# Performance work log

Hardware: AMD Instinct MI355X
Metric: run time of the kernel (lower is better)

The kernel has to match this reference:

```python
import jax, jax.numpy as jnp
import numpy as np

N_NODES = 50000
N_EDGES = 600000
N_PAIRS = 200000
F_ATOM = 64
F_PAIR = 32
HID = 128
N_LAYERS = 3
EPS = 1e-5


def setup_inputs() -> dict:
    key = jax.random.key(0)
    ks = jax.random.split(key, 24)
    d = {}
    d["atom_features"] = jax.random.normal(ks[0], (N_NODES, F_ATOM), jnp.float32)
    d["edge_index"] = jax.random.randint(ks[1], (2, N_EDGES), 0, N_NODES)
    d["pair_indices"] = jax.random.randint(ks[2], (N_PAIRS, 2), 0, N_NODES)
    d["pair_features"] = jax.random.normal(ks[3], (N_PAIRS, F_PAIR), jnp.float32)
    # atom embedding linear
    d["embed_W"] = jax.random.normal(ks[4], (F_ATOM, HID), jnp.float32) / np.sqrt(F_ATOM)
    d["embed_b"] = jnp.zeros((HID,), jnp.float32)
    # stacked GCNConv weights [L, HID, HID]
    d["conv_W"] = jax.random.normal(ks[5], (N_LAYERS, HID, HID), jnp.float32) / np.sqrt(HID)
    d["conv_b"] = jnp.zeros((N_LAYERS, HID), jnp.float32)
    # BatchNorm (eval mode: running stats)
    d["bn_gamma"] = jnp.ones((N_LAYERS, HID), jnp.float32)
    d["bn_beta"] = jnp.zeros((N_LAYERS, HID), jnp.float32)
    d["bn_mean"] = jax.random.normal(ks[6], (N_LAYERS, HID), jnp.float32) * 0.1
    d["bn_var"] = jax.random.uniform(ks[7], (N_LAYERS, HID), jnp.float32, 0.5, 1.5)
    # pair MLP: Linear(2H+Fp -> H), Linear(H -> H//2), Linear(H//2 -> 1)
    din1 = 2 * HID + F_PAIR
    d["mlp_W1"] = jax.random.normal(ks[8], (din1, HID), jnp.float32) / np.sqrt(din1)
    d["mlp_b1"] = jnp.zeros((HID,), jnp.float32)
    d["mlp_W2"] = jax.random.normal(ks[9], (HID, HID // 2), jnp.float32) / np.sqrt(HID)
    d["mlp_b2"] = jnp.zeros((HID // 2,), jnp.float32)
    d["mlp_W3"] = jax.random.normal(ks[10], (HID // 2, 1), jnp.float32) / np.sqrt(HID // 2)
    d["mlp_b3"] = jnp.zeros((1,), jnp.float32)
    return d


def _gcn_conv(x, W, b, row, col, deg_inv_sqrt):
    # PyG GCNConv: x' = W x, then symmetric-normalized sum aggregation (self-loops
    # already folded into row/col/deg_inv_sqrt).
    h = x @ W  # [N, H]
    norm = deg_inv_sqrt[row] * deg_inv_sqrt[col]  # [E']
    msg = h[col] * norm[:, None]  # [E', H] gather
    out = jax.ops.segment_sum(msg, row, num_segments=x.shape[0])  # scatter-add
    return out + b


def reference(atom_features, edge_index, pair_indices, pair_features,
              embed_W, embed_b, conv_W, conv_b,
              bn_gamma, bn_beta, bn_mean, bn_var,
              mlp_W1, mlp_b1, mlp_W2, mlp_b2, mlp_W3, mlp_b3):
    n = atom_features.shape[0]
    # add self loops once (same for every layer)
    loop = jnp.arange(n, dtype=edge_index.dtype)
    row = jnp.concatenate([edge_index[0], loop])
    col = jnp.concatenate([edge_index[1], loop])
    deg = jax.ops.segment_sum(jnp.ones_like(row, dtype=jnp.float32), row, num_segments=n)
    deg_inv_sqrt = jnp.where(deg > 0, jax.lax.rsqrt(deg), 0.0)

    x = atom_features @ embed_W + embed_b  # [N, H]
    for i in range(N_LAYERS):
        x = _gcn_conv(x, conv_W[i], conv_b[i], row, col, deg_inv_sqrt)
        # BatchNorm1d, eval mode (running stats)
        x = (x - bn_mean[i]) * jax.lax.rsqrt(bn_var[i] + EPS) * bn_gamma[i] + bn_beta[i]
        x = jax.nn.relu(x)
        # dropout: identity in eval mode

    p0 = x[pair_indices[:, 0]]  # [P, H]
    p1 = x[pair_indices[:, 1]]  # [P, H]
    z = jnp.concatenate([p0, p1, pair_features], axis=1)  # [P, 2H+Fp]
    z = jax.nn.relu(z @ mlp_W1 + mlp_b1)
    z = jax.nn.relu(z @ mlp_W2 + mlp_b2)
    return z @ mlp_W3 + mlp_b3  # [P, 1]
```

## Files before the change

kernel.cpp:

```cpp
#include <hip/hip_runtime.h>
#include <hip/hip_bf16.h>
#include <stdint.h>

#define NN 50000
#define NE 600000
#define NP 200000
#define SCAN_CHUNK 1024
#define NB_SCAN ((NN + SCAN_CHUNK - 1) / SCAN_CHUNK)

typedef __attribute__((ext_vector_type(8))) short short8;
typedef __attribute__((ext_vector_type(4))) float f32x4;

static __device__ __forceinline__ unsigned short f2bf(float f) {
  union { float f; unsigned u; } a; a.f = f;
  unsigned r = a.u + 0x7fff + ((a.u >> 16) & 1);
  return (unsigned short)(r >> 16);
}
static __device__ __forceinline__ float bf2f(unsigned short h) {
  union { unsigned u; float f; } a; a.u = ((unsigned)h) << 16;
  return a.f;
}
static __device__ __forceinline__ float lo16f(unsigned w) {
  union { unsigned u; float f; } a; a.u = w << 16; return a.f;
}
static __device__ __forceinline__ float hi16f(unsigned w) {
  union { unsigned u; float f; } a; a.u = w & 0xffff0000u; return a.f;
}


__global__ void count_kernel(const int* __restrict__ rows, int* __restrict__ counts) {
  int e = blockIdx.x * 256 + threadIdx.x;
  if (e < NE) atomicAdd(&counts[rows[e]], 1);
}

__global__ void dis_kernel(const int* __restrict__ counts, float* __restrict__ dis) {
  int i = blockIdx.x * 256 + threadIdx.x;
  if (i < NN) dis[i] = rsqrtf((float)counts[i] + 1.0f);
}

__global__ __launch_bounds__(256) void scan_partial(const int* __restrict__ counts,
                                                    int* __restrict__ bsum) {
  const int b = blockIdx.x, t = threadIdx.x;
  const int base = b * SCAN_CHUNK;
  int s = 0;
  for (int j = t; j < SCAN_CHUNK; j += 256) {
    int i = base + j;
    if (i < NN) s += counts[i];
  }
  __shared__ int red[4];
#pragma unroll
  for (int off = 32; off; off >>= 1) s += __shfl_down(s, off);
  if ((t & 63) == 0) red[t >> 6] = s;
  __syncthreads();
  if (t == 0) bsum[b] = red[0] + red[1] + red[2] + red[3];
}

__global__ void scan_mid(const int* __restrict__ bsum, int* __restrict__ bbase) {
  int t = threadIdx.x;
  int v = (t < NB_SCAN) ? bsum[t] : 0;
  int orig = v;
#pragma unroll
  for (int off = 1; off < 64; off <<= 1) {
    int u = __shfl_up(v, off);
    if (t >= off) v += u;
  }
  if (t < NB_SCAN) bbase[t] = v - orig;
}

__global__ __launch_bounds__(256) void scan_final(const int* __restrict__ counts,
                                                  const int* __restrict__ bbase,
                                                  int* __restrict__ row_ptr,
                                                  int* __restrict__ cursor) {
  const int b = blockIdx.x, t = threadIdx.x;
  const int i0 = b * SCAN_CHUNK + t * 4;
  int c[4]; int s = 0;
#pragma unroll
  for (int r = 0; r < 4; ++r) { int i = i0 + r; c[r] = (i < NN) ? counts[i] : 0; s += c[r]; }
  __shared__ int sc[256];
  sc[t] = s;
  __syncthreads();
  for (int off = 1; off < 256; off <<= 1) {
    int add = (t >= off) ? sc[t - off] : 0;
    __syncthreads();
    sc[t] += add;
    __syncthreads();
  }
  int run = bbase[b] + sc[t] - s;
#pragma unroll
  for (int r = 0; r < 4; ++r) {
    int i = i0 + r;
    if (i < NN) { row_ptr[i] = run; cursor[i] = run; run += c[r]; }
  }
  if (b == 0 && t == 0) row_ptr[NN] = NE;
}

__global__ void fill_kernel(const int* __restrict__ rows, const int* __restrict__ cols,
                            int* __restrict__ cursor, int* __restrict__ csr_col) {
  int e = blockIdx.x * 256 + threadIdx.x;
  if (e < NE) {
    int r = rows[e];
    int pos = atomicAdd(&cursor[r], 1);
    csr_col[pos] = cols[e];
  }
}


__global__ void prep_w(const float* __restrict__ embW, const float* __restrict__ convW,
                       const float* __restrict__ W1, const float* __restrict__ W2,
                       unsigned short* __restrict__ embT_hi, unsigned short* __restrict__ embT_lo,
                       unsigned short* __restrict__ convT_hi, unsigned short* __restrict__ convT_lo,
                       unsigned short* __restrict__ W1T, unsigned short* __restrict__ W2T) {
  int idx = blockIdx.x * 256 + threadIdx.x;
  if (idx < 8192) {
    int n = idx >> 6, k = idx & 63;
    float v = embW[(size_t)k * 128 + n];
    unsigned short h = f2bf(v);
    embT_hi[idx] = h;
    embT_lo[idx] = f2bf(v - bf2f(h));
  } else if (idx < 8192 + 49152) {
    int i2 = idx - 8192;
    int l = i2 >> 14, n = (i2 >> 7) & 127, k = i2 & 127;
    float v = convW[(size_t)l * 16384 + (size_t)k * 128 + n];
    unsigned short h = f2bf(v);
    convT_hi[i2] = h;
    convT_lo[i2] = f2bf(v - bf2f(h));
  } else if (idx < 8192 + 49152 + 36864) {
    int i3 = idx - 57344;
    int n = i3 / 288, k = i3 % 288;
    W1T[i3] = f2bf(W1[(size_t)k * 128 + n]);
  } else if (idx < 8192 + 49152 + 36864 + 8192) {
    int i4 = idx - 94208;
    int n = i4 >> 7, k = i4 & 127;
    W2T[i4] = f2bf(W2[(size_t)k * 64 + n]);
  }
}


__global__ __launch_bounds__(256) void agg3_kernel(const unsigned short* __restrict__ xsb,
    const int* __restrict__ row_ptr, const int* __restrict__ csr_col,
    const float* __restrict__ dis, unsigned short* __restrict__ y_bf) {
  const int t = threadIdx.x;
  const int n = blockIdx.x * 4 + (t >> 6);
  if (n >= NN) return;
  const int c = t & 63;
  const unsigned* xsw = (const unsigned*)xsb;

  unsigned wself = xsw[(size_t)n * 64 + c];
  float a0 = lo16f(wself), a1 = hi16f(wself);

  const int s = row_ptr[n], e = row_ptr[n + 1];
  int j = s;
  for (; j + 8 <= e; j += 8) {
    int cc[8]; unsigned ww[8];
#pragma unroll
    for (int q = 0; q < 8; ++q) cc[q] = csr_col[j + q];
#pragma unroll
    for (int q = 0; q < 8; ++q) ww[q] = xsw[(size_t)cc[q] * 64 + c];
#pragma unroll
    for (int q = 0; q < 8; ++q) { a0 += lo16f(ww[q]); a1 += hi16f(ww[q]); }
  }
  if (j + 4 <= e) {
    int cc[4]; unsigned ww[4];
#pragma unroll
    for (int q = 0; q < 4; ++q) cc[q] = csr_col[j + q];
#pragma unroll
    for (int q = 0; q < 4; ++q) ww[q] = xsw[(size_t)cc[q] * 64 + c];
#pragma unroll
    for (int q = 0; q < 4; ++q) { a0 += lo16f(ww[q]); a1 += hi16f(ww[q]); }
    j += 4;
  }
  for (; j < e; ++j) {
    unsigned w0 = xsw[(size_t)csr_col[j] * 64 + c];
    a0 += lo16f(w0);
    a1 += hi16f(w0);
  }
  float dv = dis[n];
  unsigned short h0 = f2bf(dv * a0), h1 = f2bf(dv * a1);
  ((unsigned*)y_bf)[(size_t)n * 64 + c] = (unsigned)h0 | ((unsigned)h1 << 16);
}


template<int K, int MODE, bool AF32>
__global__ __launch_bounds__(256) void mfma_gemm(
    const float* __restrict__ Af,
    const unsigned short* __restrict__ Ab,
    const unsigned short* __restrict__ BThi, const unsigned short* __restrict__ BTlo,
    const float* __restrict__ bias, const float* __restrict__ dis,
    const float* __restrict__ g, const float* __restrict__ be,
    const float* __restrict__ mn, const float* __restrict__ vr,
    unsigned short* __restrict__ outb, int M) {
  const int tid  = threadIdx.x;
  const int lane = tid & 63;
  const int w    = tid >> 6;
  const int l15  = lane & 15;
  const int khi  = (lane >> 4) * 8;
  const int rowb = blockIdx.x * 128 + w * 32;

  int ar[2];
#pragma unroll
  for (int rt = 0; rt < 2; ++rt) {
    int r = rowb + rt * 16 + l15;
    ar[rt] = (r < M) ? r : M - 1;
  }

  f32x4 acc[2][8];
#pragma unroll
  for (int rt = 0; rt < 2; ++rt)
#pragma unroll
    for (int ct = 0; ct < 8; ++ct) acc[rt][ct] = (f32x4){0.f, 0.f, 0.f, 0.f};

#pragma unroll
  for (int kb = 0; kb < K; kb += 32) {
    short8 ahi[2], alo[2];
#pragma unroll
    for (int rt = 0; rt < 2; ++rt) {
      if constexpr (AF32) {
        const float* asrc = Af + (size_t)ar[rt] * K + kb + khi;
        float4 va0 = *(const float4*)(asrc);
        float4 va1 = *(const float4*)(asrc + 4);
        float av[8] = {va0.x, va0.y, va0.z, va0.w, va1.x, va1.y, va1.z, va1.w};
#pragma unroll
        for (int j = 0; j < 8; ++j) {
          unsigned short h = f2bf(av[j]);
          ahi[rt][j] = (short)h;
          alo[rt][j] = (short)f2bf(av[j] - bf2f(h));
        }
      } else {
        ahi[rt] = *(const short8*)(Ab + (size_t)ar[rt] * K + kb + khi);
      }
    }
#pragma unroll
    for (int ct = 0; ct < 8; ++ct) {
      size_t woff = (size_t)(ct * 16 + l15) * K + kb + khi;
      short8 bhi = *(const short8*)(BThi + woff);
      short8 blo = *(const short8*)(BTlo + woff);
#pragma unroll
      for (int rt = 0; rt < 2; ++rt) {
        acc[rt][ct] = __builtin_amdgcn_mfma_f32_16x16x32_bf16(ahi[rt], bhi, acc[rt][ct], 0, 0, 0);
        if constexpr (AF32)
          acc[rt][ct] = __builtin_amdgcn_mfma_f32_16x16x32_bf16(alo[rt], bhi, acc[rt][ct], 0, 0, 0);
        acc[rt][ct] = __builtin_amdgcn_mfma_f32_16x16x32_bf16(ahi[rt], blo, acc[rt][ct], 0, 0, 0);
      }
    }
  }

#pragma unroll
  for (int rt = 0; rt < 2; ++rt) {
    const int orow0 = rowb + rt * 16 + (lane >> 4) * 4;
    float dv[4];
    if constexpr (MODE != 2) {
#pragma unroll
      for (int r = 0; r < 4; ++r) dv[r] = (orow0 + r < M) ? dis[orow0 + r] : 0.f;
    }
#pragma unroll
    for (int ct = 0; ct < 8; ++ct) {
      int col = ct * 16 + l15;
      float bb = bias[col];
      float scale = 1.f, shift = 0.f;
      if constexpr (MODE >= 1) {
        float inv = rsqrtf(vr[col] + 1e-5f);
        scale = g[col] * inv;
        shift = be[col] - mn[col] * scale;
      }
#pragma unroll
      for (int r = 0; r < 4; ++r) {
        int orow = orow0 + r;
        if (orow < M) {
          float v = acc[rt][ct][r] + bb;
          if constexpr (MODE >= 1) v = fmaxf(v * scale + shift, 0.f);
          if constexpr (MODE != 2) v *= dv[r];
          outb[(size_t)orow * 128 + col] = f2bf(v);
        }
      }
    }
  }
}


__global__ __launch_bounds__(256, 3) void mlp2_kernel(
    const unsigned short* __restrict__ xb, const int* __restrict__ pairs,
    const float* __restrict__ pf,
    const unsigned short* __restrict__ W1T, const float* __restrict__ b1,
    const unsigned short* __restrict__ W2T, const float* __restrict__ b2,
    const float* __restrict__ W3, const float* __restrict__ b3,
    float* __restrict__ out) {
  __shared__ unsigned short H1[128 * 136];

  const int tid  = threadIdx.x;
  const int lane = tid & 63;
  const int w    = tid >> 6;
  const int pb   = blockIdx.x * 128;
  const int rowbase = w * 32;
  const int l15  = lane & 15;
  const int khi  = (lane >> 4) * 8;
  const int rq   = (lane >> 4) * 4;

  int gp0 = pb + rowbase + l15;       if (gp0 >= NP) gp0 = NP - 1;
  int gp1 = pb + rowbase + 16 + l15;  if (gp1 >= NP) gp1 = NP - 1;
  const int2 pr0 = ((const int2*)pairs)[gp0];
  const int2 pr1 = ((const int2*)pairs)[gp1];

  short8 af[18];
#pragma unroll
  for (int kb = 0; kb < 4; ++kb) {
    af[kb]     = *(const short8*)(xb + (size_t)pr0.x * 128 + kb * 32 + khi);
    af[4 + kb] = *(const short8*)(xb + (size_t)pr0.y * 128 + kb * 32 + khi);
    af[9 + kb]     = *(const short8*)(xb + (size_t)pr1.x * 128 + kb * 32 + khi);
    af[9 + 4 + kb] = *(const short8*)(xb + (size_t)pr1.y * 128 + kb * 32 + khi);
  }
  {
    const float* q0 = pf + (size_t)gp0 * 32 + khi;
    const float* q1 = pf + (size_t)gp1 * 32 + khi;
    float4 u0 = *(const float4*)(q0), u1 = *(const float4*)(q0 + 4);
    float4 v0 = *(const float4*)(q1), v1 = *(const float4*)(q1 + 4);
    float fu[8] = {u0.x, u0.y, u0.z, u0.w, u1.x, u1.y, u1.z, u1.w};
    float fv[8] = {v0.x, v0.y, v0.z, v0.w, v1.x, v1.y, v1.z, v1.w};
#pragma unroll
    for (int j = 0; j < 8; ++j) {
      af[8][j]  = (short)f2bf(fu[j]);
      af[17][j] = (short)f2bf(fv[j]);
    }
  }

  f32x4 acc[2][8];
#pragma unroll
  for (int p = 0; p < 2; ++p)
#pragma unroll
    for (int c = 0; c < 8; ++c) acc[p][c] = (f32x4){0.f, 0.f, 0.f, 0.f};

#pragma unroll
  for (int kb = 0; kb < 9; ++kb) {
    const unsigned short* wrow = W1T + (size_t)kb * 32 + khi;
#pragma unroll
    for (int ct = 0; ct < 8; ++ct) {
      short8 bfrag = *(const short8*)(wrow + (size_t)(ct * 16 + l15) * 288);
      acc[0][ct] = __builtin_amdgcn_mfma_f32_16x16x32_bf16(af[kb], bfrag, acc[0][ct], 0, 0, 0);
      acc[1][ct] = __builtin_amdgcn_mfma_f32_16x16x32_bf16(af[9 + kb], bfrag, acc[1][ct], 0, 0, 0);
    }
  }

#pragma unroll
  for (int ct = 0; ct < 8; ++ct) {
    float bv = b1[ct * 16 + l15];
    int col = ct * 16 + l15;
#pragma unroll
    for (int p = 0; p < 2; ++p) {
#pragma unroll
      for (int r = 0; r < 4; ++r) {
        int row = rowbase + p * 16 + rq + r;
        float v = fmaxf(acc[p][ct][r] + bv, 0.f);
        H1[row * 136 + col] = f2bf(v);
      }
    }
  }
  __syncthreads();

  f32x4 acc2[2][4];
#pragma unroll
  for (int p = 0; p < 2; ++p)
#pragma unroll
    for (int c = 0; c < 4; ++c) acc2[p][c] = (f32x4){0.f, 0.f, 0.f, 0.f};

#pragma unroll
  for (int kb = 0; kb < 4; ++kb) {
    int ko = kb * 32 + khi;
    short8 a0 = *(const short8*)&H1[(rowbase + l15) * 136 + ko];
    short8 a1 = *(const short8*)&H1[(rowbase + 16 + l15) * 136 + ko];
    const unsigned short* wrow = W2T + (size_t)ko;
#pragma unroll
    for (int ct = 0; ct < 4; ++ct) {
      short8 bfrag = *(const short8*)(wrow + (size_t)(ct * 16 + l15) * 128);
      acc2[0][ct] = __builtin_amdgcn_mfma_f32_16x16x32_bf16(a0, bfrag, acc2[0][ct], 0, 0, 0);
      acc2[1][ct] = __builtin_amdgcn_mfma_f32_16x16x32_bf16(a1, bfrag, acc2[1][ct], 0, 0, 0);
    }
  }

  float w3v[4], b2v[4];
#pragma unroll
  for (int ct = 0; ct < 4; ++ct) {
    w3v[ct] = W3[ct * 16 + l15];
    b2v[ct] = b2[ct * 16 + l15];
  }
  float b3v = b3[0];
#pragma unroll
  for (int p = 0; p < 2; ++p) {
#pragma unroll
    for (int r = 0; r < 4; ++r) {
      float s = 0.f;
#pragma unroll
      for (int ct = 0; ct < 4; ++ct) {
        float h2 = fmaxf(acc2[p][ct][r] + b2v[ct], 0.f);
        s += h2 * w3v[ct];
      }
      s += __shfl_xor(s, 1);
      s += __shfl_xor(s, 2);
      s += __shfl_xor(s, 4);
      s += __shfl_xor(s, 8);
      int row = pb + rowbase + p * 16 + rq + r;
      if (l15 == 0 && row < NP) out[row] = s + b3v;
    }
  }
}


extern "C" void kernel_launch(void* const* d_in, const int* in_sizes, int n_in,
                              void* d_out, int out_size, void* d_ws, size_t ws_size,
                              hipStream_t stream) {
  (void)in_sizes; (void)n_in; (void)out_size; (void)ws_size;
  const float* atom  = (const float*)d_in[0];
  const int*   eidx  = (const int*)d_in[1];
  const int*   pairs = (const int*)d_in[2];
  const float* pfeat = (const float*)d_in[3];
  const float* embW  = (const float*)d_in[4];
  const float* embB  = (const float*)d_in[5];
  const float* convW = (const float*)d_in[6];
  const float* convB = (const float*)d_in[7];
  const float* bng   = (const float*)d_in[8];
  const float* bnb   = (const float*)d_in[9];
  const float* bnm   = (const float*)d_in[10];
  const float* bnv   = (const float*)d_in[11];
  const float* W1    = (const float*)d_in[12];
  const float* b1    = (const float*)d_in[13];
  const float* W2    = (const float*)d_in[14];
  const float* b2    = (const float*)d_in[15];
  const float* W3    = (const float*)d_in[16];
  const float* b3    = (const float*)d_in[17];
  float* out = (float*)d_out;

  uintptr_t base = (uintptr_t)d_ws;
  auto alloc = [&](size_t bytes) -> uintptr_t {
    uintptr_t p = base;
    base += (bytes + 255) & ~(size_t)255;
    return p;
  };
  int*   counts  = (int*)alloc((size_t)NN * 4);
  int*   row_ptr = (int*)alloc((size_t)(NN + 1) * 4);
  int*   cursor  = (int*)alloc((size_t)NN * 4);
  int*   csr_col = (int*)alloc((size_t)NE * 4);
  float* dis     = (float*)alloc((size_t)NN * 4);
  int*   bsum    = (int*)alloc(64 * 4);
  int*   bbase   = (int*)alloc(64 * 4);
  unsigned short* xs_bf = (unsigned short*)alloc((size_t)NN * 128 * 2);
  unsigned short* y_bf  = (unsigned short*)alloc((size_t)NN * 128 * 2);
  unsigned short* embT_hi  = (unsigned short*)alloc(8192 * 2);
  unsigned short* embT_lo  = (unsigned short*)alloc(8192 * 2);
  unsigned short* convT_hi = (unsigned short*)alloc(49152 * 2);
  unsigned short* convT_lo = (unsigned short*)alloc(49152 * 2);
  unsigned short* W1T      = (unsigned short*)alloc(36864 * 2);
  unsigned short* W2T      = (unsigned short*)alloc(8192 * 2);

  const int* erow = eidx;
  const int* ecol = eidx + NE;

  hipMemsetAsync(counts, 0, (size_t)NN * 4, stream);
  count_kernel<<<(NE + 255) / 256, 256, 0, stream>>>(erow, counts);
  dis_kernel<<<(NN + 255) / 256, 256, 0, stream>>>(counts, dis);
  scan_partial<<<NB_SCAN, 256, 0, stream>>>(counts, bsum);
  scan_mid<<<1, 64, 0, stream>>>(bsum, bbase);
  scan_final<<<NB_SCAN, 256, 0, stream>>>(counts, bbase, row_ptr, cursor);
  fill_kernel<<<(NE + 255) / 256, 256, 0, stream>>>(erow, ecol, cursor, csr_col);
  prep_w<<<(102400 + 255) / 256, 256, 0, stream>>>(embW, convW, W1, W2,
                                                   embT_hi, embT_lo, convT_hi, convT_lo,
                                                   W1T, W2T);

  mfma_gemm<64, 0, true><<<(NN + 127) / 128, 256, 0, stream>>>(
      atom, nullptr, embT_hi, embT_lo, embB, dis,
      nullptr, nullptr, nullptr, nullptr, xs_bf, NN);

  for (int l = 0; l < 3; ++l) {
    agg3_kernel<<<(NN + 3) / 4, 256, 0, stream>>>(xs_bf, row_ptr, csr_col, dis, y_bf);
    if (l < 2) {
      mfma_gemm<128, 1, false><<<(NN + 127) / 128, 256, 0, stream>>>(
          nullptr, y_bf,
          convT_hi + (size_t)l * 16384, convT_lo + (size_t)l * 16384,
          convB + (size_t)l * 128, dis,
          bng + (size_t)l * 128, bnb + (size_t)l * 128,
          bnm + (size_t)l * 128, bnv + (size_t)l * 128, xs_bf, NN);
    } else {
      mfma_gemm<128, 2, false><<<(NN + 127) / 128, 256, 0, stream>>>(
          nullptr, y_bf,
          convT_hi + (size_t)l * 16384, convT_lo + (size_t)l * 16384,
          convB + (size_t)l * 128, nullptr,
          bng + (size_t)l * 128, bnb + (size_t)l * 128,
          bnm + (size_t)l * 128, bnv + (size_t)l * 128, xs_bf, NN);
    }
  }

  mlp2_kernel<<<(NP + 127) / 128, 256, 0, stream>>>(xs_bf, pairs, pfeat,
                                                    W1T, b1, W2T, b2, W3, b3, out);
}
```

Before: 351.8 us.

## Fuse neighbor aggregation with layer GEMM via LDS tile per 64-node block

Merges the per-layer aggregation kernel and the following MFMA GEMM into one kernel. Each 512-thread block aggregates 64 nodes into a swizzled LDS tile, then runs the bf16 hi/lo MFMA GEMM with BatchNorm/ReLU on that tile. This removes the intermediate y buffer round-trip through global memory and three kernel launches. It uses ping-pong buffers between layers, at the cost of lower occupancy and an aggregation phase serialized per block.

```diff
diff --git a/kernel.cpp b/kernel.cpp
--- a/kernel.cpp
+++ b/kernel.cpp
@@ -136,59 +136,12 @@
 }
 
 
-__global__ __launch_bounds__(256) void agg3_kernel(const unsigned short* __restrict__ xsb,
-    const int* __restrict__ row_ptr, const int* __restrict__ csr_col,
-    const float* __restrict__ dis, unsigned short* __restrict__ y_bf) {
-  const int t = threadIdx.x;
-  const int n = blockIdx.x * 4 + (t >> 6);
-  if (n >= NN) return;
-  const int c = t & 63;
-  const unsigned* xsw = (const unsigned*)xsb;
-
-  unsigned wself = xsw[(size_t)n * 64 + c];
-  float a0 = lo16f(wself), a1 = hi16f(wself);
-
-  const int s = row_ptr[n], e = row_ptr[n + 1];
-  int j = s;
-  for (; j + 8 <= e; j += 8) {
-    int cc[8]; unsigned ww[8];
-#pragma unroll
-    for (int q = 0; q < 8; ++q) cc[q] = csr_col[j + q];
-#pragma unroll
-    for (int q = 0; q < 8; ++q) ww[q] = xsw[(size_t)cc[q] * 64 + c];
-#pragma unroll
-    for (int q = 0; q < 8; ++q) { a0 += lo16f(ww[q]); a1 += hi16f(ww[q]); }
-  }
-  if (j + 4 <= e) {
-    int cc[4]; unsigned ww[4];
-#pragma unroll
-    for (int q = 0; q < 4; ++q) cc[q] = csr_col[j + q];
-#pragma unroll
-    for (int q = 0; q < 4; ++q) ww[q] = xsw[(size_t)cc[q] * 64 + c];
-#pragma unroll
-    for (int q = 0; q < 4; ++q) { a0 += lo16f(ww[q]); a1 += hi16f(ww[q]); }
-    j += 4;
-  }
-  for (; j < e; ++j) {
-    unsigned w0 = xsw[(size_t)csr_col[j] * 64 + c];
-    a0 += lo16f(w0);
-    a1 += hi16f(w0);
-  }
-  float dv = dis[n];
-  unsigned short h0 = f2bf(dv * a0), h1 = f2bf(dv * a1);
-  ((unsigned*)y_bf)[(size_t)n * 64 + c] = (unsigned)h0 | ((unsigned)h1 << 16);
-}
-
-
-template<int K, int MODE, bool AF32>
-__global__ __launch_bounds__(256) void mfma_gemm(
+__global__ __launch_bounds__(256) void embed_gemm(
     const float* __restrict__ Af,
-    const unsigned short* __restrict__ Ab,
     const unsigned short* __restrict__ BThi, const unsigned short* __restrict__ BTlo,
     const float* __restrict__ bias, const float* __restrict__ dis,
-    const float* __restrict__ g, const float* __restrict__ be,
-    const float* __restrict__ mn, const float* __restrict__ vr,
     unsigned short* __restrict__ outb, int M) {
+  const int K = 64;
   const int tid  = threadIdx.x;
   const int lane = tid & 63;
   const int w    = tid >> 6;
@@ -214,19 +167,15 @@
     short8 ahi[2], alo[2];
 #pragma unroll
     for (int rt = 0; rt < 2; ++rt) {
-      if constexpr (AF32) {
-        const float* asrc = Af + (size_t)ar[rt] * K + kb + khi;
-        float4 va0 = *(const float4*)(asrc);
-        float4 va1 = *(const float4*)(asrc + 4);
-        float av[8] = {va0.x, va0.y, va0.z, va0.w, va1.x, va1.y, va1.z, va1.w};
-#pragma unroll
-        for (int j = 0; j < 8; ++j) {
-          unsigned short h = f2bf(av[j]);
-          ahi[rt][j] = (short)h;
-          alo[rt][j] = (short)f2bf(av[j] - bf2f(h));
-        }
-      } else {
-        ahi[rt] = *(const short8*)(Ab + (size_t)ar[rt] * K + kb + khi);
+      const float* asrc = Af + (size_t)ar[rt] * K + kb + khi;
+      float4 va0 = *(const float4*)(asrc);
+      float4 va1 = *(const float4*)(asrc + 4);
+      float av[8] = {va0.x, va0.y, va0.z, va0.w, va1.x, va1.y, va1.z, va1.w};
+#pragma unroll
+      for (int j = 0; j < 8; ++j) {
+        unsigned short h = f2bf(av[j]);
+        ahi[rt][j] = (short)h;
+        alo[rt][j] = (short)f2bf(av[j] - bf2f(h));
       }
     }
 #pragma unroll
@@ -237,8 +186,7 @@
 #pragma unroll
       for (int rt = 0; rt < 2; ++rt) {
         acc[rt][ct] = __builtin_amdgcn_mfma_f32_16x16x32_bf16(ahi[rt], bhi, acc[rt][ct], 0, 0, 0);
-        if constexpr (AF32)
-          acc[rt][ct] = __builtin_amdgcn_mfma_f32_16x16x32_bf16(alo[rt], bhi, acc[rt][ct], 0, 0, 0);
+        acc[rt][ct] = __builtin_amdgcn_mfma_f32_16x16x32_bf16(alo[rt], bhi, acc[rt][ct], 0, 0, 0);
         acc[rt][ct] = __builtin_amdgcn_mfma_f32_16x16x32_bf16(ahi[rt], blo, acc[rt][ct], 0, 0, 0);
       }
     }
@@ -248,29 +196,124 @@
   for (int rt = 0; rt < 2; ++rt) {
     const int orow0 = rowb + rt * 16 + (lane >> 4) * 4;
     float dv[4];
-    if constexpr (MODE != 2) {
-#pragma unroll
-      for (int r = 0; r < 4; ++r) dv[r] = (orow0 + r < M) ? dis[orow0 + r] : 0.f;
-    }
+#pragma unroll
+    for (int r = 0; r < 4; ++r) dv[r] = (orow0 + r < M) ? dis[orow0 + r] : 0.f;
 #pragma unroll
     for (int ct = 0; ct < 8; ++ct) {
       int col = ct * 16 + l15;
       float bb = bias[col];
-      float scale = 1.f, shift = 0.f;
-      if constexpr (MODE >= 1) {
-        float inv = rsqrtf(vr[col] + 1e-5f);
-        scale = g[col] * inv;
-        shift = be[col] - mn[col] * scale;
-      }
 #pragma unroll
       for (int r = 0; r < 4; ++r) {
         int orow = orow0 + r;
         if (orow < M) {
-          float v = acc[rt][ct][r] + bb;
-          if constexpr (MODE >= 1) v = fmaxf(v * scale + shift, 0.f);
-          if constexpr (MODE != 2) v *= dv[r];
+          float v = (acc[rt][ct][r] + bb) * dv[r];
           outb[(size_t)orow * 128 + col] = f2bf(v);
         }
+      }
+    }
+  }
+}
+
+
+template<int MODE>
+__global__ __launch_bounds__(512) void fused_layer(
+    const unsigned short* __restrict__ xsb,
+    const int* __restrict__ row_ptr, const int* __restrict__ csr_col,
+    const float* __restrict__ dis,
+    const unsigned short* __restrict__ BThi, const unsigned short* __restrict__ BTlo,
+    const float* __restrict__ bias,
+    const float* __restrict__ g, const float* __restrict__ be,
+    const float* __restrict__ mn, const float* __restrict__ vr,
+    unsigned short* __restrict__ outb) {
+  __shared__ unsigned ytile[64 * 64];
+
+  const int tid  = threadIdx.x;
+  const int w    = tid >> 6;
+  const int lane = tid & 63;
+  const int nb   = blockIdx.x * 64;
+  const unsigned* xsw = (const unsigned*)xsb;
+
+  for (int i = 0; i < 8; ++i) {
+    const int rloc = w * 8 + i;
+    const int n = nb + rloc;
+    float a0 = 0.f, a1 = 0.f;
+    if (n < NN) {
+      unsigned ws = xsw[(size_t)n * 64 + lane];
+      a0 = lo16f(ws); a1 = hi16f(ws);
+      const int s = row_ptr[n], e = row_ptr[n + 1];
+      int j = s;
+      for (; j + 8 <= e; j += 8) {
+        int cc[8]; unsigned ww[8];
+#pragma unroll
+        for (int q = 0; q < 8; ++q) cc[q] = csr_col[j + q];
+#pragma unroll
+        for (int q = 0; q < 8; ++q) ww[q] = xsw[(size_t)cc[q] * 64 + lane];
+#pragma unroll
+        for (int q = 0; q < 8; ++q) { a0 += lo16f(ww[q]); a1 += hi16f(ww[q]); }
+      }
+      if (j + 4 <= e) {
+        int cc[4]; unsigned ww[4];
+#pragma unroll
+        for (int q = 0; q < 4; ++q) cc[q] = csr_col[j + q];
+#pragma unroll
+        for (int q = 0; q < 4; ++q) ww[q] = xsw[(size_t)cc[q] * 64 + lane];
+#pragma unroll
+        for (int q = 0; q < 4; ++q) { a0 += lo16f(ww[q]); a1 += hi16f(ww[q]); }
+        j += 4;
+      }
+      for (; j < e; ++j) {
+        unsigned w0 = xsw[(size_t)csr_col[j] * 64 + lane];
+        a0 += lo16f(w0);
+        a1 += hi16f(w0);
+      }
+      float dv = dis[n];
+      a0 *= dv; a1 *= dv;
+    }
+    unsigned short h0 = f2bf(a0), h1 = f2bf(a1);
+    ytile[rloc * 64 + (lane ^ ((rloc & 15) << 2))] = (unsigned)h0 | ((unsigned)h1 << 16);
+  }
+  __syncthreads();
+
+  const int l15  = lane & 15;
+  const int k4   = lane >> 4;
+  const int r    = (w & 3) * 16 + l15;
+  const int colh = (w >> 2) * 64;
+  const int rsw  = (r & 15) << 2;
+
+  f32x4 acc[4];
+#pragma unroll
+  for (int ct = 0; ct < 4; ++ct) acc[ct] = (f32x4){0.f, 0.f, 0.f, 0.f};
+
+#pragma unroll
+  for (int kb = 0; kb < 4; ++kb) {
+    int q = kb * 4 + k4;
+    int chunk = q ^ (rsw >> 2);
+    short8 afrag = *(const short8*)&ytile[r * 64 + chunk * 4];
+#pragma unroll
+    for (int ct = 0; ct < 4; ++ct) {
+      size_t woff = (size_t)(colh + ct * 16 + l15) * 128 + kb * 32 + k4 * 8;
+      short8 bhi = *(const short8*)(BThi + woff);
+      short8 blo = *(const short8*)(BTlo + woff);
+      acc[ct] = __builtin_amdgcn_mfma_f32_16x16x32_bf16(afrag, bhi, acc[ct], 0, 0, 0);
+      acc[ct] = __builtin_amdgcn_mfma_f32_16x16x32_bf16(afrag, blo, acc[ct], 0, 0, 0);
+    }
+  }
+
+  const int orow0 = nb + (w & 3) * 16 + k4 * 4;
+#pragma unroll
+  for (int ct = 0; ct < 4; ++ct) {
+    int col = colh + ct * 16 + l15;
+    float bb = bias[col];
+    float inv = rsqrtf(vr[col] + 1e-5f);
+    float scale = g[col] * inv;
+    float shift = be[col] - mn[col] * scale;
+#pragma unroll
+    for (int rr = 0; rr < 4; ++rr) {
+      int orow = orow0 + rr;
+      if (orow < NN) {
+        float v = fmaxf((acc[ct][rr] + bb) * scale + shift, 0.f);
+        if constexpr (MODE == 1) v *= dis[orow];
+        outb[(size_t)orow * 128 + col] = f2bf(v);
       }
     }
   }
@@ -440,8 +483,8 @@
   float* dis     = (float*)alloc((size_t)NN * 4);
   int*   bsum    = (int*)alloc(64 * 4);
   int*   bbase   = (int*)alloc(64 * 4);
-  unsigned short* xs_bf = (unsigned short*)alloc((size_t)NN * 128 * 2);
-  unsigned short* y_bf  = (unsigned short*)alloc((size_t)NN * 128 * 2);
+  unsigned short* xsA = (unsigned short*)alloc((size_t)NN * 128 * 2);
+  unsigned short* xsB = (unsigned short*)alloc((size_t)NN * 128 * 2);
   unsigned short* embT_hi  = (unsigned short*)alloc(8192 * 2);
   unsigned short* embT_lo  = (unsigned short*)alloc(8192 * 2);
   unsigned short* convT_hi = (unsigned short*)alloc(49152 * 2);
@@ -463,29 +506,23 @@
                                                    embT_hi, embT_lo, convT_hi, convT_lo,
                                                    W1T, W2T);
 
-  mfma_gemm<64, 0, true><<<(NN + 127) / 128, 256, 0, stream>>>(
-      atom, nullptr, embT_hi, embT_lo, embB, dis,
-      nullptr, nullptr, nullptr, nullptr, xs_bf, NN);
-
-  for (int l = 0; l < 3; ++l) {
-    agg3_kernel<<<(NN + 3) / 4, 256, 0, stream>>>(xs_bf, row_ptr, csr_col, dis, y_bf);
-    if (l < 2) {
-      mfma_gemm<128, 1, false><<<(NN + 127) / 128, 256, 0, stream>>>(
-          nullptr, y_bf,
-          convT_hi + (size_t)l * 16384, convT_lo + (size_t)l * 16384,
-          convB + (size_t)l * 128, dis,
-          bng + (size_t)l * 128, bnb + (size_t)l * 128,
-          bnm + (size_t)l * 128, bnv + (size_t)l * 128, xs_bf, NN);
-    } else {
-      mfma_gemm<128, 2, false><<<(NN + 127) / 128, 256, 0, stream>>>(
-          nullptr, y_bf,
-          convT_hi + (size_t)l * 16384, convT_lo + (size_t)l * 16384,
-          convB + (size_t)l * 128, nullptr,
-          bng + (size_t)l * 128, bnb + (size_t)l * 128,
-          bnm + (size_t)l * 128, bnv + (size_t)l * 128, xs_bf, NN);
-    }
-  }
-
-  mlp2_kernel<<<(NP + 127) / 128, 256, 0, stream>>>(xs_bf, pairs, pfeat,
+  embed_gemm<<<(NN + 127) / 128, 256, 0, stream>>>(
+      atom, embT_hi, embT_lo, embB, dis, xsA, NN);
+
+  const int NBLK = (NN + 63) / 64;
+  fused_layer<1><<<NBLK, 512, 0, stream>>>(
+      xsA, row_ptr, csr_col, dis,
+      convT_hi + 0 * 16384, convT_lo + 0 * 16384, convB + 0 * 128,
+      bng + 0 * 128, bnb + 0 * 128, bnm + 0 * 128, bnv + 0 * 128, xsB);
+  fused_layer<1><<<NBLK, 512, 0, stream>>>(
+      xsB, row_ptr, csr_col, dis,
+      convT_hi + 1 * 16384, convT_lo + 1 * 16384, convB + 1 * 128,
+      bng + 1 * 128, bnb + 1 * 128, bnm + 1 * 128, bnv + 1 * 128, xsA);
+  fused_layer<2><<<NBLK, 512, 0, stream>>>(
+      xsA, row_ptr, csr_col, dis,
+      convT_hi + 2 * 16384, convT_lo + 2 * 16384, convB + 2 * 128,
+      bng + 2 * 128, bnb + 2 * 128, bnm + 2 * 128, bnv + 2 * 128, xsB);
+
+  mlp2_kernel<<<(NP + 127) / 128, 256, 0, stream>>>(xsB, pairs, pfeat,
                                                     W1T, b1, W2T, b2, W3, b3, out);
 }
```

New measurement: 357.8 us. No clear change (+1.7%).

## Use nontemporal gathers, predicated aggregation tail, and 512-thread MLP blocks

Applied to the files above, without the earlier changes.

The aggregation kernel now gathers neighbor rows with nontemporal loads and replaces the 4-wide plus scalar remainder with a predicated 4-wide loop. The pair MLP kernel changes from 4 waves each handling 32 rows to 8 waves each handling 16 rows at 512 threads per block. Halving the per-wave register footprint is meant to raise occupancy and hide gather latency. In exchange, the W1/W2 fragment loads are duplicated across more waves, and nontemporal hints may reduce cache reuse of node features that many edges share.

```diff
diff --git a/kernel.cpp b/kernel.cpp
--- a/kernel.cpp
+++ b/kernel.cpp
@@ -25,6 +25,12 @@
 }
 static __device__ __forceinline__ float hi16f(unsigned w) {
   union { unsigned u; float f; } a; a.u = w & 0xffff0000u; return a.f;
+}
+static __device__ __forceinline__ unsigned ntu32(const unsigned* p) {
+  return __builtin_nontemporal_load(p);
+}
+static __device__ __forceinline__ short8 nts8(const unsigned short* p) {
+  return __builtin_nontemporal_load((const short8*)p);
 }
 
 
@@ -145,7 +151,7 @@
   const int c = t & 63;
   const unsigned* xsw = (const unsigned*)xsb;
 
-  unsigned wself = xsw[(size_t)n * 64 + c];
+  unsigned wself = ntu32(&xsw[(size_t)n * 64 + c]);
   float a0 = lo16f(wself), a1 = hi16f(wself);
 
   const int s = row_ptr[n], e = row_ptr[n + 1];
@@ -155,24 +161,24 @@
 #pragma unroll
     for (int q = 0; q < 8; ++q) cc[q] = csr_col[j + q];
 #pragma unroll
-    for (int q = 0; q < 8; ++q) ww[q] = xsw[(size_t)cc[q] * 64 + c];
+    for (int q = 0; q < 8; ++q) ww[q] = ntu32(&xsw[(size_t)cc[q] * 64 + c]);
 #pragma unroll
     for (int q = 0; q < 8; ++q) { a0 += lo16f(ww[q]); a1 += hi16f(ww[q]); }
   }
-  if (j + 4 <= e) {
-    int cc[4]; unsigned ww[4];
-#pragma unroll
-    for (int q = 0; q < 4; ++q) cc[q] = csr_col[j + q];
-#pragma unroll
-    for (int q = 0; q < 4; ++q) ww[q] = xsw[(size_t)cc[q] * 64 + c];
-#pragma unroll
-    for (int q = 0; q < 4; ++q) { a0 += lo16f(ww[q]); a1 += hi16f(ww[q]); }
-    j += 4;
-  }
-  for (; j < e; ++j) {
-    unsigned w0 = xsw[(size_t)csr_col[j] * 64 + c];
-    a0 += lo16f(w0);
-    a1 += hi16f(w0);
+  for (; j < e; j += 4) {
+    int i1 = (j + 1 < e) ? j + 1 : j;
+    int i2 = (j + 2 < e) ? j + 2 : j;
+    int i3 = (j + 3 < e) ? j + 3 : j;
+    int c0 = csr_col[j], c1 = csr_col[i1], c2 = csr_col[i2], c3 = csr_col[i3];
+    unsigned w0 = ntu32(&xsw[(size_t)c0 * 64 + c]);
+    unsigned w1 = ntu32(&xsw[(size_t)c1 * 64 + c]);
+    unsigned w2 = ntu32(&xsw[(size_t)c2 * 64 + c]);
+    unsigned w3 = ntu32(&xsw[(size_t)c3 * 64 + c]);
+    w1 = (j + 1 < e) ? w1 : 0u;
+    w2 = (j + 2 < e) ? w2 : 0u;
+    w3 = (j + 3 < e) ? w3 : 0u;
+    a0 += lo16f(w0) + lo16f(w1) + lo16f(w2) + lo16f(w3);
+    a1 += hi16f(w0) + hi16f(w1) + hi16f(w2) + hi16f(w3);
   }
   float dv = dis[n];
   unsigned short h0 = f2bf(dv * a0), h1 = f2bf(dv * a1);
@@ -277,7 +283,7 @@
 }
 
 
-__global__ __launch_bounds__(256, 3) void mlp2_kernel(
+__global__ __launch_bounds__(512, 4) void mlp2_kernel(
     const unsigned short* __restrict__ xb, const int* __restrict__ pairs,
     const float* __restrict__ pf,
     const unsigned short* __restrict__ W1T, const float* __restrict__ b1,
@@ -290,43 +296,31 @@
   const int lane = tid & 63;
   const int w    = tid >> 6;
   const int pb   = blockIdx.x * 128;
-  const int rowbase = w * 32;
   const int l15  = lane & 15;
   const int khi  = (lane >> 4) * 8;
   const int rq   = (lane >> 4) * 4;
 
-  int gp0 = pb + rowbase + l15;       if (gp0 >= NP) gp0 = NP - 1;
-  int gp1 = pb + rowbase + 16 + l15;  if (gp1 >= NP) gp1 = NP - 1;
-  const int2 pr0 = ((const int2*)pairs)[gp0];
-  const int2 pr1 = ((const int2*)pairs)[gp1];
-
-  short8 af[18];
+  int gp = pb + w * 16 + l15;
+  if (gp >= NP) gp = NP - 1;
+  const int2 pr = ((const int2*)pairs)[gp];
+
+  short8 af[9];
 #pragma unroll
   for (int kb = 0; kb < 4; ++kb) {
-    af[kb]     = *(const short8*)(xb + (size_t)pr0.x * 128 + kb * 32 + khi);
-    af[4 + kb] = *(const short8*)(xb + (size_t)pr0.y * 128 + kb * 32 + khi);
-    af[9 + kb]     = *(const short8*)(xb + (size_t)pr1.x * 128 + kb * 32 + khi);
-    af[9 + 4 + kb] = *(const short8*)(xb + (size_t)pr1.y * 128 + kb * 32 + khi);
+    af[kb]     = nts8(xb + (size_t)pr.x * 128 + kb * 32 + khi);
+    af[4 + kb] = nts8(xb + (size_t)pr.y * 128 + kb * 32 + khi);
   }
   {
-    const float* q0 = pf + (size_t)gp0 * 32 + khi;
-    const float* q1 = pf + (size_t)gp1 * 32 + khi;
+    const float* q0 = pf + (size_t)gp * 32 + khi;
     float4 u0 = *(const float4*)(q0), u1 = *(const float4*)(q0 + 4);
-    float4 v0 = *(const float4*)(q1), v1 = *(const float4*)(q1 + 4);
     float fu[8] = {u0.x, u0.y, u0.z, u0.w, u1.x, u1.y, u1.z, u1.w};
-    float fv[8] = {v0.x, v0.y, v0.z, v0.w, v1.x, v1.y, v1.z, v1.w};
-#pragma unroll
-    for (int j = 0; j < 8; ++j) {
-      af[8][j]  = (short)f2bf(fu[j]);
-      af[17][j] = (short)f2bf(fv[j]);
-    }
-  }
-
-  f32x4 acc[2][8];
-#pragma unroll
-  for (int p = 0; p < 2; ++p)
-#pragma unroll
-    for (int c = 0; c < 8; ++c) acc[p][c] = (f32x4){0.f, 0.f, 0.f, 0.f};
+#pragma unroll
+    for (int j = 0; j < 8; ++j) af[8][j] = (short)f2bf(fu[j]);
+  }
+
+  f32x4 acc[8];
+#pragma unroll
+  for (int ct = 0; ct < 8; ++ct) acc[ct] = (f32x4){0.f, 0.f, 0.f, 0.f};
 
 #pragma unroll
   for (int kb = 0; kb < 9; ++kb) {
@@ -334,44 +328,35 @@
 #pragma unroll
     for (int ct = 0; ct < 8; ++ct) {
       short8 bfrag = *(const short8*)(wrow + (size_t)(ct * 16 + l15) * 288);
-      acc[0][ct] = __builtin_amdgcn_mfma_f32_16x16x32_bf16(af[kb], bfrag, acc[0][ct], 0, 0, 0);
-      acc[1][ct] = __builtin_amdgcn_mfma_f32_16x16x32_bf16(af[9 + kb], bfrag, acc[1][ct], 0, 0, 0);
+      acc[ct] = __builtin_amdgcn_mfma_f32_16x16x32_bf16(af[kb], bfrag, acc[ct], 0, 0, 0);
     }
   }
 
 #pragma unroll
   for (int ct = 0; ct < 8; ++ct) {
-    float bv = b1[ct * 16 + l15];
     int col = ct * 16 + l15;
-#pragma unroll
-    for (int p = 0; p < 2; ++p) {
-#pragma unroll
-      for (int r = 0; r < 4; ++r) {
-        int row = rowbase + p * 16 + rq + r;
-        float v = fmaxf(acc[p][ct][r] + bv, 0.f);
-        H1[row * 136 + col] = f2bf(v);
-      }
+    float bv = b1[col];
+#pragma unroll
+    for (int r = 0; r < 4; ++r) {
+      int row = w * 16 + rq + r;
+      H1[row * 136 + col] = f2bf(fmaxf(acc[ct][r] + bv, 0.f));
     }
   }
   __syncthreads();
 
-  f32x4 acc2[2][4];
-#pragma unroll
-  for (int p = 0; p < 2; ++p)
-#pragma unroll
-    for (int c = 0; c < 4; ++c) acc2[p][c] = (f32x4){0.f, 0.f, 0.f, 0.f};
+  f32x4 acc2[4];
+#pragma unroll
+  for (int ct = 0; ct < 4; ++ct) acc2[ct] = (f32x4){0.f, 0.f, 0.f, 0.f};
 
 #pragma unroll
   for (int kb = 0; kb < 4; ++kb) {
     int ko = kb * 32 + khi;
-    short8 a0 = *(const short8*)&H1[(rowbase + l15) * 136 + ko];
-    short8 a1 = *(const short8*)&H1[(rowbase + 16 + l15) * 136 + ko];
+    short8 a0 = *(const short8*)&H1[(w * 16 + l15) * 136 + ko];
     const unsigned short* wrow = W2T + (size_t)ko;
 #pragma unroll
     for (int ct = 0; ct < 4; ++ct) {
       short8 bfrag = *(const short8*)(wrow + (size_t)(ct * 16 + l15) * 128);
-      acc2[0][ct] = __builtin_amdgcn_mfma_f32_16x16x32_bf16(a0, bfrag, acc2[0][ct], 0, 0, 0);
-      acc2[1][ct] = __builtin_amdgcn_mfma_f32_16x16x32_bf16(a1, bfrag, acc2[1][ct], 0, 0, 0);
+      acc2[ct] = __builtin_amdgcn_mfma_f32_16x16x32_bf16(a0, bfrag, acc2[ct], 0, 0, 0);
     }
   }
 
@@ -383,22 +368,19 @@
   }
   float b3v = b3[0];
 #pragma unroll
-  for (int p = 0; p < 2; ++p) {
-#pragma unroll
-    for (int r = 0; r < 4; ++r) {
-      float s = 0.f;
-#pragma unroll
-      for (int ct = 0; ct < 4; ++ct) {
-        float h2 = fmaxf(acc2[p][ct][r] + b2v[ct], 0.f);
-        s += h2 * w3v[ct];
-      }
-      s += __shfl_xor(s, 1);
-      s += __shfl_xor(s, 2);
-      s += __shfl_xor(s, 4);
-      s += __shfl_xor(s, 8);
-      int row = pb + rowbase + p * 16 + rq + r;
-      if (l15 == 0 && row < NP) out[row] = s + b3v;
-    }
+  for (int r = 0; r < 4; ++r) {
+    float s = 0.f;
+#pragma unroll
+    for (int ct = 0; ct < 4; ++ct) {
+      float h2 = fmaxf(acc2[ct][r] + b2v[ct], 0.f);
+      s += h2 * w3v[ct];
+    }
+    s += __shfl_xor(s, 1);
+    s += __shfl_xor(s, 2);
+    s += __shfl_xor(s, 4);
+    s += __shfl_xor(s, 8);
+    int row = pb + w * 16 + rq + r;
+    if (l15 == 0 && row < NP) out[row] = s + b3v;
   }
 }
 
@@ -486,6 +468,6 @@
     }
   }
 
-  mlp2_kernel<<<(NP + 127) / 128, 256, 0, stream>>>(xs_bf, pairs, pfeat,
+  mlp2_kernel<<<(NP + 127) / 128, 512, 0, stream>>>(xs_bf, pairs, pfeat,
                                                     W1T, b1, W2T, b2, W3, b3, out);
 }
```

New measurement: 421.6 us. +19.8%, slower.
